# Kernel optimization log

Hardware: AMD Instinct MI355X
Metric: run time of the kernel (lower is better)

Reference implementation:

```python
import jax, jax.numpy as jnp
import numpy as np


def gcn_conv(h, edge_index, num_nodes):
    # Symmetric-normalized GCN aggregation: out[i] = sum_{(j->i)} h[j] / sqrt(deg(i)*deg(j))
    row, col = edge_index[0], edge_index[1]
    deg = jax.ops.segment_sum(jnp.ones(col.shape, dtype=h.dtype), col, num_segments=num_nodes)
    d_inv_sqrt = jnp.where(deg > 0, jax.lax.rsqrt(jnp.maximum(deg, 1.0)), 0.0)
    w = d_inv_sqrt[row] * d_inv_sqrt[col]           # [E]
    msg = h[row] * w[:, None]                        # [E, D] gather + scale
    return jax.ops.segment_sum(msg, col, num_segments=num_nodes)  # [N, D] scatter-add


def setup_inputs() -> dict:
    key = jax.random.key(0)
    k1, k2, k3, k4 = jax.random.split(key, 4)
    N, E, F_IN, F_HID, F_OUT = 100000, 1600000, 128, 64, 40
    x = jax.random.normal(k1, (N, F_IN), dtype=jnp.float32)
    edge_index = jax.random.randint(k2, (2, E), 0, N, dtype=jnp.int64)
    # xavier_uniform with gain=1.414 (as in reset_parameters); biases zero
    def xavier(k, shape, gain=1.414):
        fan_out, fan_in = shape
        a = gain * np.sqrt(6.0 / (fan_in + fan_out))
        return jax.random.uniform(k, shape, jnp.float32, -a, a)
    W1 = xavier(k3, (F_HID, F_IN))
    b1 = jnp.zeros((F_HID,), dtype=jnp.float32)
    W2 = xavier(k4, (F_OUT, F_HID))
    b2 = jnp.zeros((F_OUT,), dtype=jnp.float32)
    return {"x": x, "edge_index": edge_index, "W1": W1, "b1": b1, "W2": W2, "b2": b2}


def reference(x, edge_index, W1, b1, W2, b2):
    # GNN.forward with num_layers=2, use_mp=True, eval mode (dropout inactive)
    N = x.shape[0]
    h = x @ W1.T                      # [N, nhid]
    h = gcn_conv(h, edge_index, N)
    h = jax.nn.relu(h + b1)
    h = h @ W2.T                      # [N, nclass]
    h = gcn_conv(h, edge_index, N)
    return h + b2
```

## Files before the change

kernel.cpp:

```cpp
#include <hip/hip_runtime.h>
#include <hip/hip_fp16.h>


typedef __attribute__((ext_vector_type(8))) _Float16 half8v;
typedef __attribute__((ext_vector_type(4))) float   float4v;

__global__ void k_binfill(const int* __restrict__ ed,
                          int* __restrict__ gbincnt, unsigned* __restrict__ binbuf,
                          int E, int cap) {
  __shared__ int hist[512];
  __shared__ int cursor[512];
  __shared__ unsigned rec[4096];
  __shared__ unsigned short binv[4096];
  __shared__ int s_is64;
  int t = threadIdx.x;
  hist[t] = 0; hist[t + 256] = 0;
  if (t == 0) s_is64 = 1;
  __syncthreads();
  {
    int any = 0;
    #pragma unroll
    for (int u = 0; u < 8; ++u) {
      int idx = 2 * (t * 8 + u) + 1;
      if (idx < 2 * E && ed[idx] != 0) any = 1;
    }
    if (any) s_is64 = 0;
  }
  __syncthreads();
  const int is64 = s_is64;
  const int base = blockIdx.x * 4096;
  const int nE = min(4096, E - base);
  for (int j = t; j < nE; j += 256) {
    int e = base + j;
    int r = is64 ? ed[2 * e] : ed[e];
    int c = is64 ? ed[2 * (E + e)] : ed[E + e];
    rec[j] = (unsigned)r | ((unsigned)(c & 255) << 17);
    binv[j] = (unsigned short)(c >> 8);
    atomicAdd(&hist[c >> 8], 1);
  }
  __syncthreads();
  for (int b = t; b < 512; b += 256) {
    int h = hist[b];
    cursor[b] = h ? atomicAdd(&gbincnt[b], h) : 0;
  }
  __syncthreads();
  for (int j = t; j < nE; j += 256) {
    int bin = binv[j];
    int pos = atomicAdd(&cursor[bin], 1);
    if (pos < cap)
      binbuf[(size_t)bin * cap + pos] = rec[j];
  }
}

__global__ void k_degscat(const unsigned* __restrict__ binbuf, const int* __restrict__ gbincnt,
                          float* __restrict__ dis, int* __restrict__ rowptr,
                          int* __restrict__ srcs, int NBINS, int N, int cap) {
  __shared__ int sd[512];
  __shared__ int cnt[256];
  __shared__ int sc[256];
  __shared__ int cursor[256];
  __shared__ unsigned rec[8192];
  int t = threadIdx.x, b = blockIdx.x;
  sd[t]       = (t < NBINS)       ? min(gbincnt[t], cap)       : 0;
  sd[t + 256] = (t + 256 < NBINS) ? min(gbincnt[t + 256], cap) : 0;
  cnt[t] = 0;
  __syncthreads();
  for (int off = 1; off < 512; off <<= 1) {
    int v0 = (t >= off) ? sd[t - off] : 0;
    int v1 = sd[t + 256 - off];
    __syncthreads();
    sd[t] += v0; sd[t + 256] += v1;
    __syncthreads();
  }
  const int mybase = (b == 0) ? 0 : sd[b - 1];
  if (b == NBINS - 1 && t == 0) rowptr[N] = sd[NBINS - 1];

  int n = min(gbincnt[b], cap);
  const unsigned* buf = binbuf + (size_t)b * cap;
  for (int j = t; j < n; j += 256) {
    unsigned v = buf[j];
    rec[j] = v;
    atomicAdd(&cnt[v >> 17], 1);
  }
  __syncthreads();
  sc[t] = cnt[t];
  __syncthreads();
  for (int off = 1; off < 256; off <<= 1) {
    int v = (t >= off) ? sc[t - off] : 0;
    __syncthreads();
    sc[t] += v;
    __syncthreads();
  }
  int rp = mybase + ((t == 0) ? 0 : sc[t - 1]);
  cursor[t] = rp;
  int node = b * 256 + t;
  if (node < N) {
    int d = cnt[t];
    dis[node] = (d > 0) ? rsqrtf((float)d) : 0.f;
    rowptr[node] = rp;
  }
  __syncthreads();
  for (int j = t; j < n; j += 256) {
    unsigned v = rec[j];
    int pos = atomicAdd(&cursor[v >> 17], 1);
    srcs[pos] = (int)(v & 0x1FFFF);
  }
}

__launch_bounds__(256)
__global__ void k_gemm1_mfma(const float* __restrict__ X, const float* __restrict__ W,
                             const float* __restrict__ dis, __half* __restrict__ Y, int N) {
  __shared__ _Float16 xl[128 * 128];
  __shared__ _Float16 wl[64 * 128];
  const int t = threadIdx.x;
  const int row0 = blockIdx.x * 128;

  #pragma unroll
  for (int j = 0; j < 8; ++j) {
    int qq = t + 256 * j;
    int r = qq >> 5, k4 = qq & 31;
    float4 v = *(const float4*)&W[(size_t)r * 128 + k4 * 4];
    _Float16 h4[4] = {(_Float16)v.x, (_Float16)v.y, (_Float16)v.z, (_Float16)v.w};
    int k = (k4 * 4) ^ ((r & 7) * 8);
    *(float2*)&wl[r * 128 + k] = *(float2*)h4;
  }
  #pragma unroll
  for (int j = 0; j < 16; ++j) {
    int qq = t + 256 * j;
    int r = qq >> 5, k4 = qq & 31;
    int row = row0 + r;
    float4 v = make_float4(0.f, 0.f, 0.f, 0.f);
    if (row < N) v = *(const float4*)&X[(size_t)row * 128 + k4 * 4];
    _Float16 h4[4] = {(_Float16)v.x, (_Float16)v.y, (_Float16)v.z, (_Float16)v.w};
    int k = (k4 * 4) ^ ((r & 7) * 8);
    *(float2*)&xl[r * 128 + k] = *(float2*)h4;
  }
  __syncthreads();

  const int w = t >> 6, l = t & 63;
  const int m0 = w * 32;
  const int lr = l & 15, q = l >> 4;

  float4v acc[2][4] = {};
  #pragma unroll
  for (int kc = 0; kc < 4; ++kc) {
    half8v a[2], b[4];
    #pragma unroll
    for (int mt = 0; mt < 2; ++mt) {
      int m = m0 + mt * 16 + lr;
      int k = (kc * 32 + q * 8) ^ ((m & 7) * 8);
      a[mt] = *(half8v*)&xl[m * 128 + k];
    }
    #pragma unroll
    for (int nt = 0; nt < 4; ++nt) {
      int n = nt * 16 + lr;
      int k = (kc * 32 + q * 8) ^ ((n & 7) * 8);
      b[nt] = *(half8v*)&wl[n * 128 + k];
    }
    #pragma unroll
    for (int mt = 0; mt < 2; ++mt)
      #pragma unroll
      for (int nt = 0; nt < 4; ++nt)
        acc[mt][nt] = __builtin_amdgcn_mfma_f32_16x16x32_f16(a[mt], b[nt], acc[mt][nt], 0, 0, 0);
  }

  #pragma unroll
  for (int mt = 0; mt < 2; ++mt) {
    #pragma unroll
    for (int r = 0; r < 4; ++r) {
      int row = row0 + m0 + mt * 16 + q * 4 + r;
      if (row < N) {
        float dr = dis[row];
        #pragma unroll
        for (int nt = 0; nt < 4; ++nt)
          Y[(size_t)row * 64 + nt * 16 + lr] = __float2half_rn(acc[mt][nt][r] * dr);
      }
    }
  }
}

__launch_bounds__(256)
__global__ void k_gemm2_mfma(const __half* __restrict__ Xh, const float* __restrict__ W,
                             const float* __restrict__ dis, unsigned char* __restrict__ h2,
                             int N) {
  __shared__ _Float16 xl[128 * 64];
  __shared__ _Float16 wl[48 * 64];
  const int t = threadIdx.x;
  const int row0 = blockIdx.x * 128;

  for (int i = t; i < 48 * 8; i += 256) {
    int c = i >> 3, kq = i & 7;
    _Float16 h8[8];
    #pragma unroll
    for (int j = 0; j < 8; ++j)
      h8[j] = (c < 40) ? (_Float16)W[c * 64 + kq * 8 + j] : (_Float16)0.f;
    *(float4*)&wl[c * 64 + ((kq * 8) ^ ((c & 7) * 8))] = *(float4*)h8;
  }
  for (int i = t; i < 1024; i += 256) {
    int r = i >> 3, kq = i & 7;
    int row = row0 + r;
    float4 v = make_float4(0.f, 0.f, 0.f, 0.f);
    if (row < N) v = *(const float4*)&Xh[(size_t)row * 64 + kq * 8];
    *(float4*)&xl[r * 64 + ((kq * 8) ^ ((r & 7) * 8))] = v;
  }
  __syncthreads();

  const int w = t >> 6, l = t & 63;
  const int m0 = w * 32;
  const int lr = l & 15, q = l >> 4;

  float4v acc[2][3] = {};
  #pragma unroll
  for (int kc = 0; kc < 2; ++kc) {
    half8v a[2], b[3];
    #pragma unroll
    for (int mt = 0; mt < 2; ++mt) {
      int m = m0 + mt * 16 + lr;
      int k = (kc * 32 + q * 8) ^ ((m & 7) * 8);
      a[mt] = *(half8v*)&xl[m * 64 + k];
    }
    #pragma unroll
    for (int nt = 0; nt < 3; ++nt) {
      int n = nt * 16 + lr;
      int k = (kc * 32 + q * 8) ^ ((n & 7) * 8);
      b[nt] = *(half8v*)&wl[n * 64 + k];
    }
    #pragma unroll
    for (int mt = 0; mt < 2; ++mt)
      #pragma unroll
      for (int nt = 0; nt < 3; ++nt)
        acc[mt][nt] = __builtin_amdgcn_mfma_f32_16x16x32_f16(a[mt], b[nt], acc[mt][nt], 0, 0, 0);
  }

  #pragma unroll
  for (int mt = 0; mt < 2; ++mt) {
    #pragma unroll
    for (int r = 0; r < 4; ++r) {
      int row = row0 + m0 + mt * 16 + q * 4 + r;
      if (row < N) {
        float dr = dis[row];
        float v0 = acc[mt][0][r] * dr;
        float v1 = acc[mt][1][r] * dr;
        float v2 = acc[mt][2][r] * dr;
        float m = fmaxf(fabsf(v0), fmaxf(fabsf(v1), fabsf(v2)));
        #pragma unroll
        for (int off = 1; off < 16; off <<= 1)
          m = fmaxf(m, __shfl_xor(m, off));
        float s = m * (1.f / 127.f);
        float inv = (m > 0.f) ? (127.f / m) : 0.f;
        unsigned char* dst = h2 + (size_t)row * 64;
        int q0 = (int)rintf(v0 * inv);
        int q1 = (int)rintf(v1 * inv);
        int q2 = (int)rintf(v2 * inv);
        q0 = max(-127, min(127, q0));
        q1 = max(-127, min(127, q1));
        q2 = max(-127, min(127, q2));
        dst[lr]      = (unsigned char)(signed char)q0;
        dst[lr + 16] = (unsigned char)(signed char)q1;
        if (lr + 32 < 40) dst[lr + 32] = (unsigned char)(signed char)q2;
        if (lr == 0) *(float*)&dst[40] = s;
        if (lr >= 1 && lr <= 5) *(int*)&dst[40 + 4 * lr] = 0;
      }
    }
  }
}

__launch_bounds__(256)
__global__ void k_conv64(const __half* __restrict__ H, const int* __restrict__ rowptr,
                         const int* __restrict__ srcs, const float* __restrict__ dis,
                         const float* __restrict__ b1, __half* __restrict__ out, int N) {
  int node = blockIdx.x * 4 + (threadIdx.x >> 6);
  if (node >= N) return;
  int lane = threadIdx.x & 63;
  int g = lane >> 3, li = lane & 7;
  int s = rowptr[node], e = rowptr[node + 1];
  int last = e - 1;
  float a0 = 0.f, a1 = 0.f, a2 = 0.f, a3 = 0.f,
        a4 = 0.f, a5 = 0.f, a6 = 0.f, a7 = 0.f;
  for (int p = s; p < e; p += 32) {
    int sv = srcs[min(p + (lane & 31), last)];
    #pragma unroll
    for (int u = 0; u < 4; ++u) {
      int src = __shfl(sv, 8 * u + g);
      float4 raw = *(const float4*)&H[(size_t)src * 64 + 8 * li];
      if (p + 8 * u + g < e) {
        const __half2* hp = (const __half2*)&raw;
        float2 f0 = __half22float2(hp[0]);
        float2 f1 = __half22float2(hp[1]);
        float2 f2 = __half22float2(hp[2]);
        float2 f3 = __half22float2(hp[3]);
        a0 += f0.x; a1 += f0.y; a2 += f1.x; a3 += f1.y;
        a4 += f2.x; a5 += f2.y; a6 += f3.x; a7 += f3.y;
      }
    }
  }
  #pragma unroll
  for (int off = 8; off <= 32; off <<= 1) {
    a0 += __shfl_xor(a0, off); a1 += __shfl_xor(a1, off);
    a2 += __shfl_xor(a2, off); a3 += __shfl_xor(a3, off);
    a4 += __shfl_xor(a4, off); a5 += __shfl_xor(a5, off);
    a6 += __shfl_xor(a6, off); a7 += __shfl_xor(a7, off);
  }
  if (g == 0) {
    float dn = dis[node];
    const float* bb = b1 + 8 * li;
    __half hv[8];
    hv[0] = __float2half_rn(fmaxf(fmaf(a0, dn, bb[0]), 0.f));
    hv[1] = __float2half_rn(fmaxf(fmaf(a1, dn, bb[1]), 0.f));
    hv[2] = __float2half_rn(fmaxf(fmaf(a2, dn, bb[2]), 0.f));
    hv[3] = __float2half_rn(fmaxf(fmaf(a3, dn, bb[3]), 0.f));
    hv[4] = __float2half_rn(fmaxf(fmaf(a4, dn, bb[4]), 0.f));
    hv[5] = __float2half_rn(fmaxf(fmaf(a5, dn, bb[5]), 0.f));
    hv[6] = __float2half_rn(fmaxf(fmaf(a6, dn, bb[6]), 0.f));
    hv[7] = __float2half_rn(fmaxf(fmaf(a7, dn, bb[7]), 0.f));
    *(float4*)&out[(size_t)node * 64 + 8 * li] = *(float4*)hv;
  }
}

__launch_bounds__(256)
__global__ void k_conv40(const unsigned char* __restrict__ H, const int* __restrict__ rowptr,
                         const int* __restrict__ srcs, const float* __restrict__ dis,
                         const float* __restrict__ b2, float* __restrict__ out, int N) {
  int node = blockIdx.x * 4 + (threadIdx.x >> 6);
  if (node >= N) return;
  int lane = threadIdx.x & 63;
  int g = lane >> 3, li = lane & 7;
  bool act = li < 5;
  int s = rowptr[node], e = rowptr[node + 1];
  int last = e - 1;
  float a0 = 0.f, a1 = 0.f, a2 = 0.f, a3 = 0.f,
        a4 = 0.f, a5 = 0.f, a6 = 0.f, a7 = 0.f;
  for (int p = s; p < e; p += 32) {
    int sv = srcs[min(p + (lane & 31), last)];
    #pragma unroll
    for (int u = 0; u < 4; ++u) {
      int src = __shfl(sv, 8 * u + g);
      if (act) {
        const unsigned char* rowp = &H[(size_t)src * 64];
        uint2 raw = *(const uint2*)&rowp[8 * li];
        float sc = *(const float*)&rowp[40];
        if (p + 8 * u + g < e) {
          int x0 = (int)raw.x, x1 = (int)raw.y;
          a0 = fmaf((float)((x0 << 24) >> 24), sc, a0);
          a1 = fmaf((float)((x0 << 16) >> 24), sc, a1);
          a2 = fmaf((float)((x0 << 8)  >> 24), sc, a2);
          a3 = fmaf((float)( x0        >> 24), sc, a3);
          a4 = fmaf((float)((x1 << 24) >> 24), sc, a4);
          a5 = fmaf((float)((x1 << 16) >> 24), sc, a5);
          a6 = fmaf((float)((x1 << 8)  >> 24), sc, a6);
          a7 = fmaf((float)( x1        >> 24), sc, a7);
        }
      }
    }
  }
  #pragma unroll
  for (int off = 8; off <= 32; off <<= 1) {
    a0 += __shfl_xor(a0, off); a1 += __shfl_xor(a1, off);
    a2 += __shfl_xor(a2, off); a3 += __shfl_xor(a3, off);
    a4 += __shfl_xor(a4, off); a5 += __shfl_xor(a5, off);
    a6 += __shfl_xor(a6, off); a7 += __shfl_xor(a7, off);
  }
  if (g == 0 && act) {
    float dn = dis[node];
    const float* bb = b2 + 8 * li;
    float4 v0 = make_float4(fmaf(a0, dn, bb[0]), fmaf(a1, dn, bb[1]),
                            fmaf(a2, dn, bb[2]), fmaf(a3, dn, bb[3]));
    float4 v1 = make_float4(fmaf(a4, dn, bb[4]), fmaf(a5, dn, bb[5]),
                            fmaf(a6, dn, bb[6]), fmaf(a7, dn, bb[7]));
    *(float4*)&out[(size_t)node * 40 + 8 * li] = v0;
    *(float4*)&out[(size_t)node * 40 + 8 * li + 4] = v1;
  }
}

extern "C" void kernel_launch(void* const* d_in, const int* in_sizes, int n_in,
                              void* d_out, int out_size, void* d_ws, size_t ws_size,
                              hipStream_t stream) {
  const float* x  = (const float*)d_in[0];
  const int*   ed = (const int*)d_in[1];
  const float* W1 = (const float*)d_in[2];
  const float* b1 = (const float*)d_in[3];
  const float* W2 = (const float*)d_in[4];
  const float* b2 = (const float*)d_in[5];
  float* out = (float*)d_out;

  const int FIN = 128, FH = 64;
  const int N = in_sizes[0] / FIN;
  const int E = in_sizes[1] / 2;
  const int NBINS = (N + 255) >> 8;

  char* ws = (char*)d_ws;
  size_t off = 0;
  auto alloc = [&](size_t bytes) {
    void* p = ws + off;
    off = (off + bytes + 255) & ~(size_t)255;
    return p;
  };
  int*           gbincnt = (int*)alloc(512 * 4);
  float*         dis     = (float*)alloc((size_t)N * 4);
  int*           rowptr  = (int*)alloc(((size_t)N + 1) * 4);
  int*           srcs    = (int*)alloc((size_t)E * 4);
  __half*        h1      = (__half*)alloc((size_t)N * FH * 2);
  __half*        h1b     = (__half*)alloc((size_t)N * FH * 2);
  unsigned char* h2      = (unsigned char*)alloc((size_t)N * 64);
  int cap = (int)(((size_t)N * FH * 2) / ((size_t)NBINS * 4));
  if (cap > 8192) cap = 8192;
  unsigned* binbuf = (unsigned*)h1;

  hipMemsetAsync(gbincnt, 0, 512 * 4, stream);

  int fb = (E + 4095) / 4096;
  k_binfill<<<fb, 256, 0, stream>>>(ed, gbincnt, binbuf, E, cap);
  k_degscat<<<NBINS, 256, 0, stream>>>(binbuf, gbincnt, dis, rowptr, srcs, NBINS, N, cap);

  int mb = (N + 127) / 128;
  int cb = (N + 3) / 4;
  k_gemm1_mfma<<<mb, 256, 0, stream>>>(x, W1, dis, h1, N);
  k_conv64<<<cb, 256, 0, stream>>>(h1, rowptr, srcs, dis, b1, h1b, N);
  k_gemm2_mfma<<<mb, 256, 0, stream>>>(h1b, W2, dis, h2, N);
  k_conv40<<<cb, 256, 0, stream>>>(h2, rowptr, srcs, dis, b2, out, N);
}
```

Before: 253.0 us.

## Quantize first-layer features to int8 with per-row scale for aggregation

The first GEMM now writes its output as int8 with a per-row float scale, found by a max-reduction across the 16 lanes that share a row, in place of fp16. The first aggregation kernel dequantizes these on the fly, which halves the bytes gathered per edge in the memory-bound scatter phase. Both aggregation kernels also stop their unrolled inner loop early when the remaining edge slots lie past the node's end, avoiding wasted gathers. The trade is a loss of accuracy in layer-one activations and an extra scale load per edge from a separate array.

After: 253.7 us. No clear change (+0.3%).

```diff
diff --git a/kernel.cpp b/kernel.cpp
--- a/kernel.cpp
+++ b/kernel.cpp
@@ -109,7 +109,8 @@
 
 __launch_bounds__(256)
 __global__ void k_gemm1_mfma(const float* __restrict__ X, const float* __restrict__ W,
-                             const float* __restrict__ dis, __half* __restrict__ Y, int N) {
+                             const float* __restrict__ dis, unsigned char* __restrict__ h1q,
+                             float* __restrict__ sc1, int N) {
   __shared__ _Float16 xl[128 * 128];
   __shared__ _Float16 wl[64 * 128];
   const int t = threadIdx.x;
@@ -171,9 +172,29 @@
       int row = row0 + m0 + mt * 16 + q * 4 + r;
       if (row < N) {
         float dr = dis[row];
+        float v0 = acc[mt][0][r] * dr;
+        float v1 = acc[mt][1][r] * dr;
+        float v2 = acc[mt][2][r] * dr;
+        float v3 = acc[mt][3][r] * dr;
+        float m = fmaxf(fmaxf(fabsf(v0), fabsf(v1)), fmaxf(fabsf(v2), fabsf(v3)));
         #pragma unroll
-        for (int nt = 0; nt < 4; ++nt)
-          Y[(size_t)row * 64 + nt * 16 + lr] = __float2half_rn(acc[mt][nt][r] * dr);
+        for (int off = 1; off < 16; off <<= 1)
+          m = fmaxf(m, __shfl_xor(m, off));
+        float inv = (m > 0.f) ? (127.f / m) : 0.f;
+        unsigned char* dst = h1q + (size_t)row * 64;
+        int q0 = (int)rintf(v0 * inv);
+        int q1 = (int)rintf(v1 * inv);
+        int q2 = (int)rintf(v2 * inv);
+        int q3 = (int)rintf(v3 * inv);
+        q0 = max(-127, min(127, q0));
+        q1 = max(-127, min(127, q1));
+        q2 = max(-127, min(127, q2));
+        q3 = max(-127, min(127, q3));
+        dst[lr]      = (unsigned char)(signed char)q0;
+        dst[lr + 16] = (unsigned char)(signed char)q1;
+        dst[lr + 32] = (unsigned char)(signed char)q2;
+        dst[lr + 48] = (unsigned char)(signed char)q3;
+        if (lr == 0) sc1[row] = m * (1.f / 127.f);
       }
     }
   }
@@ -266,9 +287,10 @@
 }
 
 __launch_bounds__(256)
-__global__ void k_conv64(const __half* __restrict__ H, const int* __restrict__ rowptr,
-                         const int* __restrict__ srcs, const float* __restrict__ dis,
-                         const float* __restrict__ b1, __half* __restrict__ out, int N) {
+__global__ void k_conv64(const unsigned char* __restrict__ H, const float* __restrict__ sc1,
+                         const int* __restrict__ rowptr, const int* __restrict__ srcs,
+                         const float* __restrict__ dis, const float* __restrict__ b1,
+                         __half* __restrict__ out, int N) {
   int node = blockIdx.x * 4 + (threadIdx.x >> 6);
   if (node >= N) return;
   int lane = threadIdx.x & 63;
@@ -281,16 +303,20 @@
     int sv = srcs[min(p + (lane & 31), last)];
     #pragma unroll
     for (int u = 0; u < 4; ++u) {
+      if (p + 8 * u >= e) break;
       int src = __shfl(sv, 8 * u + g);
-      float4 raw = *(const float4*)&H[(size_t)src * 64 + 8 * li];
+      uint2 raw = *(const uint2*)&H[(size_t)src * 64 + 8 * li];
+      float sc = sc1[src];
       if (p + 8 * u + g < e) {
-        const __half2* hp = (const __half2*)&raw;
-        float2 f0 = __half22float2(hp[0]);
-        float2 f1 = __half22float2(hp[1]);
-        float2 f2 = __half22float2(hp[2]);
-        float2 f3 = __half22float2(hp[3]);
-        a0 += f0.x; a1 += f0.y; a2 += f1.x; a3 += f1.y;
-        a4 += f2.x; a5 += f2.y; a6 += f3.x; a7 += f3.y;
+        int x0 = (int)raw.x, x1 = (int)raw.y;
+        a0 = fmaf((float)((x0 << 24) >> 24), sc, a0);
+        a1 = fmaf((float)((x0 << 16) >> 24), sc, a1);
+        a2 = fmaf((float)((x0 << 8)  >> 24), sc, a2);
+        a3 = fmaf((float)( x0        >> 24), sc, a3);
+        a4 = fmaf((float)((x1 << 24) >> 24), sc, a4);
+        a5 = fmaf((float)((x1 << 16) >> 24), sc, a5);
+        a6 = fmaf((float)((x1 << 8)  >> 24), sc, a6);
+        a7 = fmaf((float)( x1        >> 24), sc, a7);
       }
     }
   }
@@ -334,6 +360,7 @@
     int sv = srcs[min(p + (lane & 31), last)];
     #pragma unroll
     for (int u = 0; u < 4; ++u) {
+      if (p + 8 * u >= e) break;
       int src = __shfl(sv, 8 * u + g);
       if (act) {
         const unsigned char* rowp = &H[(size_t)src * 64];
@@ -399,12 +426,13 @@
   float*         dis     = (float*)alloc((size_t)N * 4);
   int*           rowptr  = (int*)alloc(((size_t)N + 1) * 4);
   int*           srcs    = (int*)alloc((size_t)E * 4);
-  __half*        h1      = (__half*)alloc((size_t)N * FH * 2);
+  unsigned char* h1q     = (unsigned char*)alloc((size_t)N * FH * 2);
   __half*        h1b     = (__half*)alloc((size_t)N * FH * 2);
   unsigned char* h2      = (unsigned char*)alloc((size_t)N * 64);
+  float* sc1 = (float*)(h1q + (((size_t)N * 64 + 255) & ~(size_t)255));
   int cap = (int)(((size_t)N * FH * 2) / ((size_t)NBINS * 4));
   if (cap > 8192) cap = 8192;
-  unsigned* binbuf = (unsigned*)h1;
+  unsigned* binbuf = (unsigned*)h1q;
 
   hipMemsetAsync(gbincnt, 0, 512 * 4, stream);
 
@@ -414,8 +442,8 @@
 
   int mb = (N + 127) / 128;
   int cb = (N + 3) / 4;
-  k_gemm1_mfma<<<mb, 256, 0, stream>>>(x, W1, dis, h1, N);
-  k_conv64<<<cb, 256, 0, stream>>>(h1, rowptr, srcs, dis, b1, h1b, N);
+  k_gemm1_mfma<<<mb, 256, 0, stream>>>(x, W1, dis, h1q, sc1, N);
+  k_conv64<<<cb, 256, 0, stream>>>(h1q, sc1, rowptr, srcs, dis, b1, h1b, N);
   k_gemm2_mfma<<<mb, 256, 0, stream>>>(h1b, W2, dis, h2, N);
   k_conv40<<<cb, 256, 0, stream>>>(h2, rowptr, srcs, dis, b2, out, N);
 }
```
